# Kernel optimization log

Measured on AMD Instinct MI355X. Metric: run time of the kernel, lower is better.

## Reference

```python
import jax, jax.numpy as jnp
import numpy as np

N = 50000      # nodes
E = 800000     # edges (before self loops)
F_IN = 64      # n_features
H = 4          # heads
EPS = 1e-5


def _feast_conv(x, src, dst, W, u, c, b, out_ch):
    # FeaStConv (PyG): q_h = softmax_h(u_h^T (x_j - x_i) + c_h);
    # x_i' = mean_{j in N(i)} sum_h q_h * (W_h x_j) + b
    xs = x[src]                                   # [E', Fin]
    xd = x[dst]                                   # [E', Fin]
    q = jax.nn.softmax((xs - xd) @ u + c, axis=-1)          # [E', H]
    m = (xs @ W).reshape(xs.shape[0], H, out_ch)            # [E', H, out]
    msg = jnp.einsum('eh,eho->eo', q, m)                    # [E', out]
    num = jax.ops.segment_sum(msg, dst, num_segments=N)     # [N, out]
    deg = jax.ops.segment_sum(jnp.ones((msg.shape[0],), msg.dtype), dst, num_segments=N)
    return num / jnp.clip(deg, 1.0)[:, None] + b


def setup_inputs() -> dict:
    key = jax.random.key(0)
    ks = jax.random.split(key, 32)
    def gn(k, shape, s=0.1):
        return jax.random.normal(k, shape, jnp.float32) * s
    inp = {
        'x': jax.random.normal(ks[0], (N, F_IN), jnp.float32),
        'edge_index': jax.random.randint(ks[1], (2, E), 0, N),
        # FeaStConv 1: 64 -> 16
        'W1': gn(ks[2], (F_IN, H * 16)), 'u1': gn(ks[3], (F_IN, H)),
        'c1': gn(ks[4], (H,)), 'b1': gn(ks[5], (16,)),
        # FeaStConv 2: 16 -> 32
        'W2': gn(ks[6], (16, H * 32)), 'u2': gn(ks[7], (16, H)),
        'c2': gn(ks[8], (H,)), 'b2': gn(ks[9], (32,)),
        # FeaStConv 3: 32 -> 64
        'W3': gn(ks[10], (32, H * 64)), 'u3': gn(ks[11], (32, H)),
        'c3': gn(ks[12], (H,)), 'b3': gn(ks[13], (64,)),
        # BatchNorm(64) affine params (training-mode batch stats)
        'gamma': jnp.ones((64,), jnp.float32), 'beta': jnp.zeros((64,), jnp.float32),
        # MLP head
        'lw1': gn(ks[14], (64, 32)), 'lb1': gn(ks[15], (32,)),
        'lw2': gn(ks[16], (32, 16)), 'lb2': gn(ks[17], (16,)),
        'lw3': gn(ks[18], (16, 8)),  'lb3': gn(ks[19], (8,)),
        'lw4': gn(ks[20], (8, 4)),   'lb4': gn(ks[21], (4,)),
        'ow':  gn(ks[22], (4, 1)),   'ob':  gn(ks[23], (1,)),
    }
    return inp


def reference(x, edge_index, W1, u1, c1, b1, W2, u2, c2, b2, W3, u3, c3, b3,
              gamma, beta, lw1, lb1, lw2, lb2, lw3, lb3, lw4, lb4, ow, ob):
    # add self loops (PyG FeaStConv default)
    loops = jnp.arange(N, dtype=edge_index.dtype)
    src = jnp.concatenate([edge_index[0], loops])
    dst = jnp.concatenate([edge_index[1], loops])

    h = jax.nn.relu(_feast_conv(x, src, dst, W1, u1, c1, b1, 16))
    h = jax.nn.relu(_feast_conv(h, src, dst, W2, u2, c2, b2, 32))
    h = jax.nn.relu(_feast_conv(h, src, dst, W3, u3, c3, b3, 64))

    # BatchNorm over node dim (training-mode biased batch stats)
    mu = h.mean(axis=0)
    var = h.var(axis=0)
    h = (h - mu) * jax.lax.rsqrt(var + EPS) * gamma + beta

    h = jax.nn.relu(h @ lw1 + lb1)
    h = jax.nn.relu(h @ lw2 + lb2)
    h = jax.nn.relu(h @ lw3 + lb3)
    h = jax.nn.relu(h @ lw4 + lb4)
    return jax.nn.sigmoid(h @ ow + ob)    # [N, 1]
```

## Files before the change

### kernel.cpp

```cpp
#include <hip/hip_runtime.h>

#define NNODES 50000
#define NEDGES 800000
#define SCAN_BLOCKS ((NNODES + 255) / 256)
#define NPART (NNODES / 8)
#define EPS 2048
#define NSLICE ((NEDGES + EPS - 1) / EPS)

__device__ __forceinline__ float4 softq(float4 ss, float4 sd, float4 c4) {
  float l0 = ss.x - sd.x + c4.x;
  float l1 = ss.y - sd.y + c4.y;
  float l2 = ss.z - sd.z + c4.z;
  float l3 = ss.w - sd.w + c4.w;
  float mx = fmaxf(fmaxf(l0, l1), fmaxf(l2, l3));
  float e0 = __expf(l0 - mx), e1 = __expf(l1 - mx);
  float e2 = __expf(l2 - mx), e3 = __expf(l3 - mx);
  float inv = 1.f / (e0 + e1 + e2 + e3);
  return make_float4(e0 * inv, e1 * inv, e2 * inv, e3 * inv);
}

__device__ __forceinline__ void fma4(float4& a, float q, float4 v) {
  a.x += q * v.x; a.y += q * v.y; a.z += q * v.z; a.w += q * v.w;
}
__device__ __forceinline__ float dot4(float4 a, float4 b) {
  return a.x * b.x + a.y * b.y + a.z * b.z + a.w * b.w;
}

__global__ __launch_bounds__(256) void hist_kernel(const int* __restrict__ ei,
                                                   int* __restrict__ counts,
                                                   int* __restrict__ rank) {
  int e = blockIdx.x * 256 + threadIdx.x;
  if (e < NEDGES) rank[e] = atomicAdd(&counts[ei[NEDGES + e]], 1);
}

__global__ __launch_bounds__(256) void scanA_kernel(const int* __restrict__ counts,
                                                    int* __restrict__ rowptr,
                                                    int* __restrict__ blockSum) {
  __shared__ int sm[256];
  int i = blockIdx.x * 256 + threadIdx.x;
  int v = (i < NNODES) ? counts[i] : 0;
  sm[threadIdx.x] = v;
  __syncthreads();
  for (int off = 1; off < 256; off <<= 1) {
    int x = (threadIdx.x >= off) ? sm[threadIdx.x - off] : 0;
    __syncthreads();
    sm[threadIdx.x] += x;
    __syncthreads();
  }
  if (i < NNODES) rowptr[i] = sm[threadIdx.x] - v;
  if (threadIdx.x == 255) blockSum[blockIdx.x] = sm[255];
}

__global__ __launch_bounds__(256) void scanB_kernel(int* __restrict__ blockSum,
                                                    int* __restrict__ blockOff) {
  __shared__ int sm[256];
  int v = (threadIdx.x < SCAN_BLOCKS) ? blockSum[threadIdx.x] : 0;
  sm[threadIdx.x] = v;
  __syncthreads();
  for (int off = 1; off < 256; off <<= 1) {
    int x = (threadIdx.x >= off) ? sm[threadIdx.x - off] : 0;
    __syncthreads();
    sm[threadIdx.x] += x;
    __syncthreads();
  }
  if (threadIdx.x < SCAN_BLOCKS) blockOff[threadIdx.x] = sm[threadIdx.x] - v;
}

__global__ __launch_bounds__(256) void scanC_kernel(int* __restrict__ rowptr,
                                                    const int* __restrict__ blockOff) {
  int i = blockIdx.x * 256 + threadIdx.x;
  if (i < NNODES) rowptr[i] += blockOff[blockIdx.x];
  if (i == 0) rowptr[NNODES] = NEDGES;
}

__global__ __launch_bounds__(256) void scatter_kernel(const int* __restrict__ ei,
                                                      const int* __restrict__ rowptr,
                                                      const int* __restrict__ rank,
                                                      int* __restrict__ col) {
  const int p = blockIdx.x & 7;
  const int sl = blockIdx.x >> 3;
  const int P0 = p * NPART;
  const int e1 = min((sl + 1) * EPS, NEDGES);
  for (int e = sl * EPS + threadIdx.x; e < e1; e += 256) {
    int dst = __builtin_nontemporal_load(&ei[NEDGES + e]);
    if ((unsigned)(dst - P0) < (unsigned)NPART) {
      int pos = rowptr[dst] + __builtin_nontemporal_load(&rank[e]);
      col[pos] = __builtin_nontemporal_load(&ei[e]);
    }
  }
}

__global__ __launch_bounds__(256) void prep_kernel(const float* __restrict__ W1,
                                                   const float* __restrict__ W2,
                                                   const float* __restrict__ W3,
                                                   float* __restrict__ Wk1,
                                                   float* __restrict__ Wk2,
                                                   float* __restrict__ Wk3) {
  int i = blockIdx.x * 256 + threadIdx.x;
  if (i < 4096) {
    int f = i >> 6, j = i & 63;
    Wk1[i] = W1[f * 64 + ((j & 3) << 4) + (j >> 2)];
  } else if (i < 6144) {
    int i2 = i - 4096;
    int k = i2 >> 5, o = i2 & 31;
    int hh = k >> 4, f = k & 15;
    Wk2[i2] = W2[f * 128 + hh * 32 + o];
  } else if (i < 14336) {
    int i3 = i - 6144;
    int k = i3 >> 6, o = i3 & 63;
    int hh = k >> 5, f = k & 31;
    Wk3[i3] = W3[f * 256 + hh * 64 + o];
  }
}

template<int K, int OUTT, int MO, bool DEGBIAS>
__global__ __launch_bounds__(256) void ngemm_kernel(const float* __restrict__ A,
                                                    const float* __restrict__ Wk,
                                                    const int* __restrict__ rowptr,
                                                    const float* __restrict__ bptr,
                                                    float* __restrict__ C) {
  constexpr int OG = OUTT / MO;
  constexpr int NB = 256 / OG;
  constexpr int NBp = NB + 1;
  __shared__ float ldsT[K * NBp];
  const int tid = threadIdx.x;
  const int nb0 = blockIdx.x * NB;
  for (int i = tid; i < NB * (K / 4); i += 256) {
    int r = i / (K / 4), kq = i - r * (K / 4);
    int n = nb0 + r;
    if (n >= NNODES) n = NNODES - 1;
    float4 v = *(const float4*)(A + (size_t)n * K + (kq << 2));
    ldsT[((kq << 2) + 0) * NBp + r] = v.x;
    ldsT[((kq << 2) + 1) * NBp + r] = v.y;
    ldsT[((kq << 2) + 2) * NBp + r] = v.z;
    ldsT[((kq << 2) + 3) * NBp + r] = v.w;
  }
  __syncthreads();
  const int o0 = __builtin_amdgcn_readfirstlane(tid / NB) * MO;
  const int nl = tid & (NB - 1);
  const int n = nb0 + nl;
  float acc[MO];
#pragma unroll
  for (int m = 0; m < MO; ++m) acc[m] = 0.f;
#pragma unroll 4
  for (int k = 0; k < K; ++k) {
    float a = ldsT[k * NBp + nl];
    const float* wr = Wk + k * OUTT + o0;
#pragma unroll
    for (int m = 0; m < MO; ++m) acc[m] += a * wr[m];
  }
  if (n < NNODES) {
    float sc = 1.f;
    if (DEGBIAS) sc = 1.f / (float)(rowptr[n + 1] - rowptr[n] + 1);
#pragma unroll
    for (int m4 = 0; m4 < MO / 4; ++m4) {
      float4 v;
      if (DEGBIAS) {
        v.x = fmaxf(acc[m4 * 4 + 0] * sc + bptr[o0 + m4 * 4 + 0], 0.f);
        v.y = fmaxf(acc[m4 * 4 + 1] * sc + bptr[o0 + m4 * 4 + 1], 0.f);
        v.z = fmaxf(acc[m4 * 4 + 2] * sc + bptr[o0 + m4 * 4 + 2], 0.f);
        v.w = fmaxf(acc[m4 * 4 + 3] * sc + bptr[o0 + m4 * 4 + 3], 0.f);
      } else {
        v = make_float4(acc[m4 * 4 + 0], acc[m4 * 4 + 1],
                        acc[m4 * 4 + 2], acc[m4 * 4 + 3]);
      }
      *(float4*)(C + (size_t)n * OUTT + o0 + m4 * 4) = v;
    }
  }
}

template<int FIN>
__global__ __launch_bounds__(256) void s_kernel(const float* __restrict__ x,
                                                const float* __restrict__ u,
                                                float* __restrict__ s) {
  int tid = blockIdx.x * 256 + threadIdx.x;
  int n = tid >> 2, h = tid & 3;
  if (n >= NNODES) return;
  const float4* xr = (const float4*)(x + (size_t)n * FIN);
  float acc = 0.f;
#pragma unroll
  for (int f4 = 0; f4 < FIN / 4; ++f4) {
    float4 xv = xr[f4];
    acc += xv.x * u[(4 * f4 + 0) * 4 + h] + xv.y * u[(4 * f4 + 1) * 4 + h] +
           xv.z * u[(4 * f4 + 2) * 4 + h] + xv.w * u[(4 * f4 + 3) * 4 + h];
  }
  s[tid] = acc;
}

__global__ __launch_bounds__(256) void gather1_kernel(const int* __restrict__ rowptr,
                                                      const int* __restrict__ col,
                                                      const float* __restrict__ s,
                                                      const float* __restrict__ t,
                                                      const float* __restrict__ cptr,
                                                      const float* __restrict__ bptr,
                                                      float* __restrict__ h) {
  const int lane = threadIdx.x & 7;
  const int sub = threadIdx.x >> 3;
  const int n = blockIdx.x * 32 + sub;
  if (n >= NNODES) return;
  float4 c4 = *(const float4*)cptr;
  float mxc = fmaxf(fmaxf(c4.x, c4.y), fmaxf(c4.z, c4.w));
  float4 qs = make_float4(__expf(c4.x - mxc), __expf(c4.y - mxc),
                          __expf(c4.z - mxc), __expf(c4.w - mxc));
  float sinv = 1.f / (qs.x + qs.y + qs.z + qs.w);
  qs.x *= sinv; qs.y *= sinv; qs.z *= sinv; qs.w *= sinv;
  float4 sd = *(const float4*)(s + 4 * (size_t)n);
  const float4* trow = (const float4*)(t + (size_t)n * 64);
  float acc0 = dot4(qs, trow[2 * lane + 0]);
  float acc1 = dot4(qs, trow[2 * lane + 1]);
  const int beg = rowptr[n], end = rowptr[n + 1];
  int idx = beg;
  for (; idx + 3 < end; idx += 4) {
    int s0 = col[idx], s1 = col[idx + 1], s2 = col[idx + 2], s3 = col[idx + 3];
    float4 a0 = *(const float4*)(s + 4 * (size_t)s0);
    float4 a1 = *(const float4*)(s + 4 * (size_t)s1);
    float4 a2 = *(const float4*)(s + 4 * (size_t)s2);
    float4 a3 = *(const float4*)(s + 4 * (size_t)s3);
    const float4* t0 = (const float4*)(t + (size_t)s0 * 64) + 2 * lane;
    const float4* t1 = (const float4*)(t + (size_t)s1 * 64) + 2 * lane;
    const float4* t2 = (const float4*)(t + (size_t)s2 * 64) + 2 * lane;
    const float4* t3 = (const float4*)(t + (size_t)s3 * 64) + 2 * lane;
    float4 u0 = t0[0], v0 = t0[1];
    float4 u1 = t1[0], v1 = t1[1];
    float4 u2 = t2[0], v2 = t2[1];
    float4 u3 = t3[0], v3 = t3[1];
    float4 q0 = softq(a0, sd, c4);
    float4 q1 = softq(a1, sd, c4);
    float4 q2 = softq(a2, sd, c4);
    float4 q3 = softq(a3, sd, c4);
    acc0 += dot4(q0, u0) + dot4(q1, u1) + dot4(q2, u2) + dot4(q3, u3);
    acc1 += dot4(q0, v0) + dot4(q1, v1) + dot4(q2, v2) + dot4(q3, v3);
  }
  for (; idx < end; ++idx) {
    int src = col[idx];
    float4 qv = softq(*(const float4*)(s + 4 * (size_t)src), sd, c4);
    const float4* tw = (const float4*)(t + (size_t)src * 64) + 2 * lane;
    acc0 += dot4(qv, tw[0]);
    acc1 += dot4(qv, tw[1]);
  }
  float d = 1.f / (float)(end - beg + 1);
  h[(size_t)n * 16 + 2 * lane + 0] = fmaxf(acc0 * d + bptr[2 * lane + 0], 0.f);
  h[(size_t)n * 16 + 2 * lane + 1] = fmaxf(acc1 * d + bptr[2 * lane + 1], 0.f);
}

template<int FIN>
__global__ __launch_bounds__(256) void gatherG_kernel(const int* __restrict__ rowptr,
                                                      const int* __restrict__ col,
                                                      const float* __restrict__ s,
                                                      const float* __restrict__ x,
                                                      const float* __restrict__ cptr,
                                                      float* __restrict__ g) {
  constexpr int LPN = FIN / 4;
  constexpr int NSUB = 256 / LPN;
  const int lane = threadIdx.x & (LPN - 1);
  const int sub = threadIdx.x / LPN;
  const int n = blockIdx.x * NSUB + sub;
  if (n >= NNODES) return;
  float4 c4 = *(const float4*)cptr;
  float mxc = fmaxf(fmaxf(c4.x, c4.y), fmaxf(c4.z, c4.w));
  float4 qsl = make_float4(__expf(c4.x - mxc), __expf(c4.y - mxc),
                           __expf(c4.z - mxc), __expf(c4.w - mxc));
  float sinv = 1.f / (qsl.x + qsl.y + qsl.z + qsl.w);
  qsl.x *= sinv; qsl.y *= sinv; qsl.z *= sinv; qsl.w *= sinv;
  float4 sd = *(const float4*)(s + 4 * (size_t)n);
  float4 xn = *((const float4*)(x + (size_t)n * FIN) + lane);
  float4 g0 = make_float4(qsl.x * xn.x, qsl.x * xn.y, qsl.x * xn.z, qsl.x * xn.w);
  float4 g1 = make_float4(qsl.y * xn.x, qsl.y * xn.y, qsl.y * xn.z, qsl.y * xn.w);
  float4 g2 = make_float4(qsl.z * xn.x, qsl.z * xn.y, qsl.z * xn.z, qsl.z * xn.w);
  float4 g3 = make_float4(qsl.w * xn.x, qsl.w * xn.y, qsl.w * xn.z, qsl.w * xn.w);
  const int beg = rowptr[n], end = rowptr[n + 1];
  int idx = beg;
  for (; idx + 3 < end; idx += 4) {
    int s0 = col[idx], s1 = col[idx + 1], s2 = col[idx + 2], s3 = col[idx + 3];
    float4 a0 = *(const float4*)(s + 4 * (size_t)s0);
    float4 a1 = *(const float4*)(s + 4 * (size_t)s1);
    float4 a2 = *(const float4*)(s + 4 * (size_t)s2);
    float4 a3 = *(const float4*)(s + 4 * (size_t)s3);
    float4 x0 = *((const float4*)(x + (size_t)s0 * FIN) + lane);
    float4 x1 = *((const float4*)(x + (size_t)s1 * FIN) + lane);
    float4 x2 = *((const float4*)(x + (size_t)s2 * FIN) + lane);
    float4 x3 = *((const float4*)(x + (size_t)s3 * FIN) + lane);
    float4 q0 = softq(a0, sd, c4);
    float4 q1 = softq(a1, sd, c4);
    float4 q2 = softq(a2, sd, c4);
    float4 q3 = softq(a3, sd, c4);
    fma4(g0, q0.x, x0); fma4(g1, q0.y, x0); fma4(g2, q0.z, x0); fma4(g3, q0.w, x0);
    fma4(g0, q1.x, x1); fma4(g1, q1.y, x1); fma4(g2, q1.z, x1); fma4(g3, q1.w, x1);
    fma4(g0, q2.x, x2); fma4(g1, q2.y, x2); fma4(g2, q2.z, x2); fma4(g3, q2.w, x2);
    fma4(g0, q3.x, x3); fma4(g1, q3.y, x3); fma4(g2, q3.z, x3); fma4(g3, q3.w, x3);
  }
  for (; idx < end; ++idx) {
    int src = col[idx];
    float4 qv = softq(*(const float4*)(s + 4 * (size_t)src), sd, c4);
    float4 xv = *((const float4*)(x + (size_t)src * FIN) + lane);
    fma4(g0, qv.x, xv); fma4(g1, qv.y, xv); fma4(g2, qv.z, xv); fma4(g3, qv.w, xv);
  }
  float* gr = g + (size_t)n * 4 * FIN;
  *(float4*)(gr + 0 * FIN + 4 * lane) = g0;
  *(float4*)(gr + 1 * FIN + 4 * lane) = g1;
  *(float4*)(gr + 2 * FIN + 4 * lane) = g2;
  *(float4*)(gr + 3 * FIN + 4 * lane) = g3;
}

__global__ __launch_bounds__(256) void stats_kernel(const float* __restrict__ h3,
                                                    float* __restrict__ sums) {
  const int o = threadIdx.x & 63;
  const int r = threadIdx.x >> 6;
  float accS = 0.f, accQ = 0.f;
  for (int base = blockIdx.x * 4; base < NNODES; base += gridDim.x * 4) {
    int n = base + r;
    if (n < NNODES) {
      float v = h3[(size_t)n * 64 + o];
      accS += v;
      accQ += v * v;
    }
  }
  __shared__ float ls[256], lq[256];
  ls[threadIdx.x] = accS;
  lq[threadIdx.x] = accQ;
  __syncthreads();
  if (threadIdx.x < 64) {
    float a = ls[threadIdx.x] + ls[threadIdx.x + 64] + ls[threadIdx.x + 128] + ls[threadIdx.x + 192];
    float qq = lq[threadIdx.x] + lq[threadIdx.x + 64] + lq[threadIdx.x + 128] + lq[threadIdx.x + 192];
    atomicAdd(&sums[threadIdx.x], a);
    atomicAdd(&sums[64 + threadIdx.x], qq);
  }
}

__global__ __launch_bounds__(256) void mlp_kernel(
    const float* __restrict__ h3, const float* __restrict__ sums,
    const float* __restrict__ gamma, const float* __restrict__ beta,
    const float* __restrict__ lw1, const float* __restrict__ lb1,
    const float* __restrict__ lw2, const float* __restrict__ lb2,
    const float* __restrict__ lw3, const float* __restrict__ lb3,
    const float* __restrict__ lw4, const float* __restrict__ lb4,
    const float* __restrict__ ow, const float* __restrict__ ob,
    float* __restrict__ out) {
  __shared__ float w1[64 * 32], w2[32 * 16], w3[16 * 8], w4[8 * 4];
  __shared__ float b1s[32], b2s[16], b3s[8], b4s[4], wos[4];
  __shared__ float scale[64], shift[64];
  int tid = threadIdx.x;
  for (int i = tid; i < 64 * 32; i += 256) w1[i] = lw1[i];
  for (int i = tid; i < 32 * 16; i += 256) w2[i] = lw2[i];
  if (tid < 128) w3[tid] = lw3[tid];
  if (tid < 32) { w4[tid] = lw4[tid]; b1s[tid] = lb1[tid]; }
  if (tid < 16) b2s[tid] = lb2[tid];
  if (tid < 8) b3s[tid] = lb3[tid];
  if (tid < 4) { b4s[tid] = lb4[tid]; wos[tid] = ow[tid]; }
  if (tid < 64) {
    float mu = sums[tid] * (1.f / NNODES);
    float var = sums[64 + tid] * (1.f / NNODES) - mu * mu;
    float sc = rsqrtf(var + 1e-5f) * gamma[tid];
    scale[tid] = sc;
    shift[tid] = beta[tid] - mu * sc;
  }
  __syncthreads();
  int n = blockIdx.x * 256 + tid;
  if (n >= NNODES) return;
  float obv = ob[0];
  const float4* hr = (const float4*)(h3 + (size_t)n * 64);
  float z1[32];
#pragma unroll
  for (int j = 0; j < 32; ++j) z1[j] = b1s[j];
  for (int i4 = 0; i4 < 16; ++i4) {
    float4 hv = hr[i4];
    float a0 = hv.x * scale[4 * i4 + 0] + shift[4 * i4 + 0];
    float a1 = hv.y * scale[4 * i4 + 1] + shift[4 * i4 + 1];
    float a2 = hv.z * scale[4 * i4 + 2] + shift[4 * i4 + 2];
    float a3 = hv.w * scale[4 * i4 + 3] + shift[4 * i4 + 3];
#pragma unroll
    for (int j = 0; j < 32; ++j) {
      z1[j] += a0 * w1[(4 * i4 + 0) * 32 + j] + a1 * w1[(4 * i4 + 1) * 32 + j] +
               a2 * w1[(4 * i4 + 2) * 32 + j] + a3 * w1[(4 * i4 + 3) * 32 + j];
    }
  }
  float z2[16];
#pragma unroll
  for (int j = 0; j < 16; ++j) z2[j] = b2s[j];
  for (int i = 0; i < 32; ++i) {
    float a = fmaxf(z1[i], 0.f);
#pragma unroll
    for (int j = 0; j < 16; ++j) z2[j] += a * w2[i * 16 + j];
  }
  float z3[8];
#pragma unroll
  for (int j = 0; j < 8; ++j) z3[j] = b3s[j];
  for (int i = 0; i < 16; ++i) {
    float a = fmaxf(z2[i], 0.f);
#pragma unroll
    for (int j = 0; j < 8; ++j) z3[j] += a * w3[i * 8 + j];
  }
  float z4[4];
#pragma unroll
  for (int j = 0; j < 4; ++j) z4[j] = b4s[j];
  for (int i = 0; i < 8; ++i) {
    float a = fmaxf(z3[i], 0.f);
#pragma unroll
    for (int j = 0; j < 4; ++j) z4[j] += a * w4[i * 4 + j];
  }
  float zo = obv;
#pragma unroll
  for (int i = 0; i < 4; ++i) zo += fmaxf(z4[i], 0.f) * wos[i];
  out[n] = 1.f / (1.f + __expf(-zo));
}

extern "C" void kernel_launch(void* const* d_in, const int* in_sizes, int n_in,
                              void* d_out, int out_size, void* d_ws, size_t ws_size,
                              hipStream_t stream) {
  const float* x  = (const float*)d_in[0];
  const int*   ei = (const int*)d_in[1];
  const float* W1 = (const float*)d_in[2];  const float* u1 = (const float*)d_in[3];
  const float* c1 = (const float*)d_in[4];  const float* b1 = (const float*)d_in[5];
  const float* W2 = (const float*)d_in[6];  const float* u2 = (const float*)d_in[7];
  const float* c2 = (const float*)d_in[8];  const float* b2 = (const float*)d_in[9];
  const float* W3 = (const float*)d_in[10]; const float* u3 = (const float*)d_in[11];
  const float* c3 = (const float*)d_in[12]; const float* b3 = (const float*)d_in[13];
  const float* gamma = (const float*)d_in[14]; const float* beta = (const float*)d_in[15];
  const float* lw1 = (const float*)d_in[16]; const float* lb1 = (const float*)d_in[17];
  const float* lw2 = (const float*)d_in[18]; const float* lb2 = (const float*)d_in[19];
  const float* lw3 = (const float*)d_in[20]; const float* lb3 = (const float*)d_in[21];
  const float* lw4 = (const float*)d_in[22]; const float* lb4 = (const float*)d_in[23];
  const float* ow  = (const float*)d_in[24]; const float* ob  = (const float*)d_in[25];
  float* out = (float*)d_out;

  float* t    = (float*)d_ws;
  float* g    = t + (size_t)NNODES * 64;
  float* hA   = g + (size_t)NNODES * 128;
  float* hB   = hA + (size_t)NNODES * 64;
  float* s    = hB + (size_t)NNODES * 64;
  float* sums = s + (size_t)NNODES * 4;
  float* Wk1  = sums + 128;
  float* Wk2  = Wk1 + 4096;
  float* Wk3  = Wk2 + 2048;
  int*   rowptr   = (int*)(Wk3 + 8192);
  int*   counts   = rowptr + NNODES + 8;
  int*   blockSum = counts + NNODES;
  int*   blockOff = blockSum + 256;
  int*   col      = blockOff + 256;
  int*   rank     = col + NEDGES;

  hipMemsetAsync(counts, 0, NNODES * sizeof(int), stream);
  hipMemsetAsync(sums, 0, 128 * sizeof(float), stream);

  prep_kernel<<<56, 256, 0, stream>>>(W1, W2, W3, Wk1, Wk2, Wk3);
  hist_kernel<<<(NEDGES + 255) / 256, 256, 0, stream>>>(ei, counts, rank);
  scanA_kernel<<<SCAN_BLOCKS, 256, 0, stream>>>(counts, rowptr, blockSum);
  scanB_kernel<<<1, 256, 0, stream>>>(blockSum, blockOff);
  scanC_kernel<<<SCAN_BLOCKS, 256, 0, stream>>>(rowptr, blockOff);
  scatter_kernel<<<NSLICE * 8, 256, 0, stream>>>(ei, rowptr, rank, col);

  ngemm_kernel<64, 64, 16, false><<<(NNODES + 63) / 64, 256, 0, stream>>>(x, Wk1, nullptr, nullptr, t);
  s_kernel<64><<<(NNODES * 4 + 255) / 256, 256, 0, stream>>>(x, u1, s);
  gather1_kernel<<<(NNODES + 31) / 32, 256, 0, stream>>>(rowptr, col, s, t, c1, b1, hA);

  s_kernel<16><<<(NNODES * 4 + 255) / 256, 256, 0, stream>>>(hA, u2, s);
  gatherG_kernel<16><<<(NNODES + 63) / 64, 256, 0, stream>>>(rowptr, col, s, hA, c2, g);
  ngemm_kernel<64, 32, 16, true><<<(NNODES + 127) / 128, 256, 0, stream>>>(g, Wk2, rowptr, b2, hB);

  s_kernel<32><<<(NNODES * 4 + 255) / 256, 256, 0, stream>>>(hB, u3, s);
  gatherG_kernel<32><<<(NNODES + 31) / 32, 256, 0, stream>>>(rowptr, col, s, hB, c3, g);
  ngemm_kernel<128, 64, 16, true><<<(NNODES + 63) / 64, 256, 0, stream>>>(g, Wk3, rowptr, b3, hA);

  stats_kernel<<<256, 256, 0, stream>>>(hA, sums);
  mlp_kernel<<<(NNODES + 255) / 256, 256, 0, stream>>>(hA, sums, gamma, beta, lw1, lb1,
                                                       lw2, lb2, lw3, lb3, lw4, lb4,
                                                       ow, ob, out);
}
```

Baseline: 266.3 us.

## Fuse softmax-weighted gather with per-node GEMM for layers two and three

After: 245.4 us. -7.9%, faster.

```diff
diff --git a/kernel.cpp b/kernel.cpp
--- a/kernel.cpp
+++ b/kernel.cpp
@@ -24,6 +24,12 @@
 }
 __device__ __forceinline__ float dot4(float4 a, float4 b) {
   return a.x * b.x + a.y * b.y + a.z * b.z + a.w * b.w;
+}
+__device__ __forceinline__ void st4T(float* ldsT, int k0, int NBp, int nl, float4 v) {
+  ldsT[(k0 + 0) * NBp + nl] = v.x;
+  ldsT[(k0 + 1) * NBp + nl] = v.y;
+  ldsT[(k0 + 2) * NBp + nl] = v.z;
+  ldsT[(k0 + 3) * NBp + nl] = v.w;
 }
 
 __global__ __launch_bounds__(256) void hist_kernel(const int* __restrict__ ei,
@@ -130,10 +136,7 @@
     int n = nb0 + r;
     if (n >= NNODES) n = NNODES - 1;
     float4 v = *(const float4*)(A + (size_t)n * K + (kq << 2));
-    ldsT[((kq << 2) + 0) * NBp + r] = v.x;
-    ldsT[((kq << 2) + 1) * NBp + r] = v.y;
-    ldsT[((kq << 2) + 2) * NBp + r] = v.z;
-    ldsT[((kq << 2) + 3) * NBp + r] = v.w;
+    st4T(ldsT, kq << 2, NBp, r, v);
   }
   __syncthreads();
   const int o0 = __builtin_amdgcn_readfirstlane(tid / NB) * MO;
@@ -165,6 +168,113 @@
                         acc[m4 * 4 + 2], acc[m4 * 4 + 3]);
       }
       *(float4*)(C + (size_t)n * OUTT + o0 + m4 * 4) = v;
+    }
+  }
+}
+
+template<int FIN, int OUTT, int MO>
+__global__ __launch_bounds__(256) void fusedG_kernel(const int* __restrict__ rowptr,
+                                                     const int* __restrict__ col,
+                                                     const float* __restrict__ s,
+                                                     const float* __restrict__ x,
+                                                     const float* __restrict__ Wk,
+                                                     const float* __restrict__ cptr,
+                                                     const float* __restrict__ bptr,
+                                                     float* __restrict__ h) {
+  constexpr int LPN = FIN / 8;
+  constexpr int NB = 256 / LPN;
+  constexpr int NBp = NB + 1;
+  constexpr int K = 4 * FIN;
+  constexpr int OG = OUTT / MO;
+  static_assert(OG == 256 / NB, "geometry mismatch");
+  __shared__ float ldsT[K * NBp];
+  const int tid = threadIdx.x;
+  const int nb0 = blockIdx.x * NB;
+
+  {
+    const int lane = tid & (LPN - 1);
+    const int sub = tid / LPN;
+    int n = nb0 + sub;
+    if (n >= NNODES) n = NNODES - 1;
+    float4 c4 = *(const float4*)cptr;
+    float mxc = fmaxf(fmaxf(c4.x, c4.y), fmaxf(c4.z, c4.w));
+    float4 qsl = make_float4(__expf(c4.x - mxc), __expf(c4.y - mxc),
+                             __expf(c4.z - mxc), __expf(c4.w - mxc));
+    float sinv = 1.f / (qsl.x + qsl.y + qsl.z + qsl.w);
+    qsl.x *= sinv; qsl.y *= sinv; qsl.z *= sinv; qsl.w *= sinv;
+    float4 sd = *(const float4*)(s + 4 * (size_t)n);
+    const float4* xn = (const float4*)(x + (size_t)n * FIN) + 2 * lane;
+    float4 xa = xn[0], xb = xn[1];
+    float4 g0a = make_float4(qsl.x * xa.x, qsl.x * xa.y, qsl.x * xa.z, qsl.x * xa.w);
+    float4 g0b = make_float4(qsl.x * xb.x, qsl.x * xb.y, qsl.x * xb.z, qsl.x * xb.w);
+    float4 g1a = make_float4(qsl.y * xa.x, qsl.y * xa.y, qsl.y * xa.z, qsl.y * xa.w);
+    float4 g1b = make_float4(qsl.y * xb.x, qsl.y * xb.y, qsl.y * xb.z, qsl.y * xb.w);
+    float4 g2a = make_float4(qsl.z * xa.x, qsl.z * xa.y, qsl.z * xa.z, qsl.z * xa.w);
+    float4 g2b = make_float4(qsl.z * xb.x, qsl.z * xb.y, qsl.z * xb.z, qsl.z * xb.w);
+    float4 g3a = make_float4(qsl.w * xa.x, qsl.w * xa.y, qsl.w * xa.z, qsl.w * xa.w);
+    float4 g3b = make_float4(qsl.w * xb.x, qsl.w * xb.y, qsl.w * xb.z, qsl.w * xb.w);
+    const int beg = rowptr[n], end = rowptr[n + 1];
+    int idx = beg;
+    for (; idx + 1 < end; idx += 2) {
+      int s0 = col[idx], s1 = col[idx + 1];
+      float4 a0 = *(const float4*)(s + 4 * (size_t)s0);
+      float4 a1 = *(const float4*)(s + 4 * (size_t)s1);
+      const float4* xr0 = (const float4*)(x + (size_t)s0 * FIN) + 2 * lane;
+      const float4* xr1 = (const float4*)(x + (size_t)s1 * FIN) + 2 * lane;
+      float4 x0a = xr0[0], x0b = xr0[1];
+      float4 x1a = xr1[0], x1b = xr1[1];
+      float4 q0 = softq(a0, sd, c4);
+      float4 q1 = softq(a1, sd, c4);
+      fma4(g0a, q0.x, x0a); fma4(g0b, q0.x, x0b);
+      fma4(g1a, q0.y, x0a); fma4(g1b, q0.y, x0b);
+      fma4(g2a, q0.z, x0a); fma4(g2b, q0.z, x0b);
+      fma4(g3a, q0.w, x0a); fma4(g3b, q0.w, x0b);
+      fma4(g0a, q1.x, x1a); fma4(g0b, q1.x, x1b);
+      fma4(g1a, q1.y, x1a); fma4(g1b, q1.y, x1b);
+      fma4(g2a, q1.z, x1a); fma4(g2b, q1.z, x1b);
+      fma4(g3a, q1.w, x1a); fma4(g3b, q1.w, x1b);
+    }
+    if (idx < end) {
+      int s0 = col[idx];
+      float4 qv = softq(*(const float4*)(s + 4 * (size_t)s0), sd, c4);
+      const float4* xr0 = (const float4*)(x + (size_t)s0 * FIN) + 2 * lane;
+      float4 x0a = xr0[0], x0b = xr0[1];
+      fma4(g0a, qv.x, x0a); fma4(g0b, qv.x, x0b);
+      fma4(g1a, qv.y, x0a); fma4(g1b, qv.y, x0b);
+      fma4(g2a, qv.z, x0a); fma4(g2b, qv.z, x0b);
+      fma4(g3a, qv.w, x0a); fma4(g3b, qv.w, x0b);
+    }
+    const int f0 = 8 * lane;
+    st4T(ldsT, 0 * FIN + f0, NBp, sub, g0a); st4T(ldsT, 0 * FIN + f0 + 4, NBp, sub, g0b);
+    st4T(ldsT, 1 * FIN + f0, NBp, sub, g1a); st4T(ldsT, 1 * FIN + f0 + 4, NBp, sub, g1b);
+    st4T(ldsT, 2 * FIN + f0, NBp, sub, g2a); st4T(ldsT, 2 * FIN + f0 + 4, NBp, sub, g2b);
+    st4T(ldsT, 3 * FIN + f0, NBp, sub, g3a); st4T(ldsT, 3 * FIN + f0 + 4, NBp, sub, g3b);
+  }
+  __syncthreads();
+
+  const int o0 = __builtin_amdgcn_readfirstlane(tid / NB) * MO;
+  const int nl = tid & (NB - 1);
+  const int n = nb0 + nl;
+  float acc[MO];
+#pragma unroll
+  for (int m = 0; m < MO; ++m) acc[m] = 0.f;
+#pragma unroll 4
+  for (int k = 0; k < K; ++k) {
+    float a = ldsT[k * NBp + nl];
+    const float* wr = Wk + k * OUTT + o0;
+#pragma unroll
+    for (int m = 0; m < MO; ++m) acc[m] += a * wr[m];
+  }
+  if (n < NNODES) {
+    float sc = 1.f / (float)(rowptr[n + 1] - rowptr[n] + 1);
+#pragma unroll
+    for (int m4 = 0; m4 < MO / 4; ++m4) {
+      float4 v;
+      v.x = fmaxf(acc[m4 * 4 + 0] * sc + bptr[o0 + m4 * 4 + 0], 0.f);
+      v.y = fmaxf(acc[m4 * 4 + 1] * sc + bptr[o0 + m4 * 4 + 1], 0.f);
+      v.z = fmaxf(acc[m4 * 4 + 2] * sc + bptr[o0 + m4 * 4 + 2], 0.f);
+      v.w = fmaxf(acc[m4 * 4 + 3] * sc + bptr[o0 + m4 * 4 + 3], 0.f);
+      *(float4*)(h + (size_t)n * OUTT + o0 + m4 * 4) = v;
     }
   }
 }
@@ -243,65 +353,6 @@
   h[(size_t)n * 16 + 2 * lane + 1] = fmaxf(acc1 * d + bptr[2 * lane + 1], 0.f);
 }
 
-template<int FIN>
-__global__ __launch_bounds__(256) void gatherG_kernel(const int* __restrict__ rowptr,
-                                                      const int* __restrict__ col,
-                                                      const float* __restrict__ s,
-                                                      const float* __restrict__ x,
-                                                      const float* __restrict__ cptr,
-                                                      float* __restrict__ g) {
-  constexpr int LPN = FIN / 4;
-  constexpr int NSUB = 256 / LPN;
-  const int lane = threadIdx.x & (LPN - 1);
-  const int sub = threadIdx.x / LPN;
-  const int n = blockIdx.x * NSUB + sub;
-  if (n >= NNODES) return;
-  float4 c4 = *(const float4*)cptr;
-  float mxc = fmaxf(fmaxf(c4.x, c4.y), fmaxf(c4.z, c4.w));
-  float4 qsl = make_float4(__expf(c4.x - mxc), __expf(c4.y - mxc),
-                           __expf(c4.z - mxc), __expf(c4.w - mxc));
-  float sinv = 1.f / (qsl.x + qsl.y + qsl.z + qsl.w);
-  qsl.x *= sinv; qsl.y *= sinv; qsl.z *= sinv; qsl.w *= sinv;
-  float4 sd = *(const float4*)(s + 4 * (size_t)n);
-  float4 xn = *((const float4*)(x + (size_t)n * FIN) + lane);
-  float4 g0 = make_float4(qsl.x * xn.x, qsl.x * xn.y, qsl.x * xn.z, qsl.x * xn.w);
-  float4 g1 = make_float4(qsl.y * xn.x, qsl.y * xn.y, qsl.y * xn.z, qsl.y * xn.w);
-  float4 g2 = make_float4(qsl.z * xn.x, qsl.z * xn.y, qsl.z * xn.z, qsl.z * xn.w);
-  float4 g3 = make_float4(qsl.w * xn.x, qsl.w * xn.y, qsl.w * xn.z, qsl.w * xn.w);
-  const int beg = rowptr[n], end = rowptr[n + 1];
-  int idx = beg;
-  for (; idx + 3 < end; idx += 4) {
-    int s0 = col[idx], s1 = col[idx + 1], s2 = col[idx + 2], s3 = col[idx + 3];
-    float4 a0 = *(const float4*)(s + 4 * (size_t)s0);
-    float4 a1 = *(const float4*)(s + 4 * (size_t)s1);
-    float4 a2 = *(const float4*)(s + 4 * (size_t)s2);
-    float4 a3 = *(const float4*)(s + 4 * (size_t)s3);
-    float4 x0 = *((const float4*)(x + (size_t)s0 * FIN) + lane);
-    float4 x1 = *((const float4*)(x + (size_t)s1 * FIN) + lane);
-    float4 x2 = *((const float4*)(x + (size_t)s2 * FIN) + lane);
-    float4 x3 = *((const float4*)(x + (size_t)s3 * FIN) + lane);
-    float4 q0 = softq(a0, sd, c4);
-    float4 q1 = softq(a1, sd, c4);
-    float4 q2 = softq(a2, sd, c4);
-    float4 q3 = softq(a3, sd, c4);
-    fma4(g0, q0.x, x0); fma4(g1, q0.y, x0); fma4(g2, q0.z, x0); fma4(g3, q0.w, x0);
-    fma4(g0, q1.x, x1); fma4(g1, q1.y, x1); fma4(g2, q1.z, x1); fma4(g3, q1.w, x1);
-    fma4(g0, q2.x, x2); fma4(g1, q2.y, x2); fma4(g2, q2.z, x2); fma4(g3, q2.w, x2);
-    fma4(g0, q3.x, x3); fma4(g1, q3.y, x3); fma4(g2, q3.z, x3); fma4(g3, q3.w, x3);
-  }
-  for (; idx < end; ++idx) {
-    int src = col[idx];
-    float4 qv = softq(*(const float4*)(s + 4 * (size_t)src), sd, c4);
-    float4 xv = *((const float4*)(x + (size_t)src * FIN) + lane);
-    fma4(g0, qv.x, xv); fma4(g1, qv.y, xv); fma4(g2, qv.z, xv); fma4(g3, qv.w, xv);
-  }
-  float* gr = g + (size_t)n * 4 * FIN;
-  *(float4*)(gr + 0 * FIN + 4 * lane) = g0;
-  *(float4*)(gr + 1 * FIN + 4 * lane) = g1;
-  *(float4*)(gr + 2 * FIN + 4 * lane) = g2;
-  *(float4*)(gr + 3 * FIN + 4 * lane) = g3;
-}
-
 __global__ __launch_bounds__(256) void stats_kernel(const float* __restrict__ h3,
                                                     float* __restrict__ sums) {
   const int o = threadIdx.x & 63;
@@ -424,8 +475,7 @@
   float* out = (float*)d_out;
 
   float* t    = (float*)d_ws;
-  float* g    = t + (size_t)NNODES * 64;
-  float* hA   = g + (size_t)NNODES * 128;
+  float* hA   = t + (size_t)NNODES * 64;
   float* hB   = hA + (size_t)NNODES * 64;
   float* s    = hB + (size_t)NNODES * 64;
   float* sums = s + (size_t)NNODES * 4;
@@ -454,12 +504,10 @@
   gather1_kernel<<<(NNODES + 31) / 32, 256, 0, stream>>>(rowptr, col, s, t, c1, b1, hA);
 
   s_kernel<16><<<(NNODES * 4 + 255) / 256, 256, 0, stream>>>(hA, u2, s);
-  gatherG_kernel<16><<<(NNODES + 63) / 64, 256, 0, stream>>>(rowptr, col, s, hA, c2, g);
-  ngemm_kernel<64, 32, 16, true><<<(NNODES + 127) / 128, 256, 0, stream>>>(g, Wk2, rowptr, b2, hB);
+  fusedG_kernel<16, 32, 16><<<(NNODES + 127) / 128, 256, 0, stream>>>(rowptr, col, s, hA, Wk2, c2, b2, hB);
 
   s_kernel<32><<<(NNODES * 4 + 255) / 256, 256, 0, stream>>>(hB, u3, s);
-  gatherG_kernel<32><<<(NNODES + 31) / 32, 256, 0, stream>>>(rowptr, col, s, hB, c3, g);
-  ngemm_kernel<128, 64, 16, true><<<(NNODES + 63) / 64, 256, 0, stream>>>(g, Wk3, rowptr, b3, hA);
+  fusedG_kernel<32, 64, 16><<<(NNODES + 63) / 64, 256, 0, stream>>>(rowptr, col, s, hB, Wk3, c3, b3, hA);
 
   stats_kernel<<<256, 256, 0, stream>>>(hA, sums);
   mlp_kernel<<<(NNODES + 255) / 256, 256, 0, stream>>>(hA, sums, gamma, beta, lw1, lb1,
```
